# Kernel tuning notes

Measured on AMD Instinct MI355X. Metric: run time of the kernel, lower is better.

The kernel has to match this reference:

```python
import jax, jax.numpy as jnp
import numpy as np

IN_COUNT, OUT_COUNT, NUM_BASIS = 512, 512, 8
X_MIN, X_MAX, GAMMA_SCALE = 0.0, 1.0, 3.0
BATCH = 8192


def setup_inputs() -> dict:
    key = jax.random.key(0)
    k_x, k_c = jax.random.split(key)
    x = jax.random.uniform(k_x, (BATCH, IN_COUNT), dtype=jnp.float32)
    coeffs = 0.01 * jax.random.normal(k_c, (OUT_COUNT, IN_COUNT, NUM_BASIS), dtype=jnp.float32)
    centers_1d = jnp.linspace(X_MIN, X_MAX, NUM_BASIS, dtype=jnp.float32)
    centers = jnp.tile(centers_1d[None, :], (IN_COUNT, 1))  # (in, basis)
    delta = (X_MAX - X_MIN) / (NUM_BASIS - 1)
    gamma = GAMMA_SCALE / delta
    slopes = jnp.full((IN_COUNT, NUM_BASIS), gamma, dtype=jnp.float32)
    return {"x": x, "coeffs": coeffs, "centers": centers, "slopes": slopes}


def reference(x, coeffs, centers, slopes):
    # s_im(x) = 0.5 * (1 + tanh(gamma_im * (x_bi - c_im)))  -> (batch, in, basis)
    basis = 0.5 * (1.0 + jnp.tanh(slopes[None, :, :] * (x[:, :, None] - centers[None, :, :])))
    # y_bj = sum_{i,m} a_jim * s_bim : fused double reduction (GEMM-shaped)
    y = jnp.einsum('bim,jim->bj', basis, coeffs)
    return y
```

## Files before the change

### kernel.cpp

```cpp
#include <hip/hip_runtime.h>

#define BATCH 8192
#define INC   512
#define OUTC  512
#define NB    8
#define KDIM  (INC * NB)

#define BM 128
#define BN 128
#define BK 64
#define KSPLIT 2
#define THREADS 256
#define LDA 72

typedef __attribute__((ext_vector_type(8))) short bf16x8;
typedef __attribute__((ext_vector_type(4))) float f32x4;
typedef __attribute__((ext_vector_type(4))) int   i32x4;

static __device__ __forceinline__ unsigned int pk2(float lo, float hi) {
    return __builtin_amdgcn_perm(__builtin_bit_cast(unsigned int, hi),
                                 __builtin_bit_cast(unsigned int, lo),
                                 0x07060302u);
}

__global__ __launch_bounds__(256)
void w_prepass(const float* __restrict__ W, unsigned short* __restrict__ Wb,
               float* __restrict__ Y) {
    const int gid  = blockIdx.x * 256 + threadIdx.x;
    const int base = gid * 8;
    const float4 a = *(const float4*)(W + base);
    const float4 b = *(const float4*)(W + base + 4);
    const float v[8] = {a.x, a.y, a.z, a.w, b.x, b.y, b.z, b.w};
    unsigned int r[8];
#pragma unroll
    for (int i = 0; i < 8; ++i) {
        unsigned int t = __builtin_bit_cast(unsigned int, v[i]);
        t += 0x7FFFu + ((t >> 16) & 1u);
        r[i] = t >> 16;
    }
    i32x4 out = {(int)(r[0] | (r[1] << 16)), (int)(r[2] | (r[3] << 16)),
                 (int)(r[4] | (r[5] << 16)), (int)(r[6] | (r[7] << 16))};
    *(i32x4*)(Wb + base) = out;

    float4* yp = (float4*)Y + (size_t)gid * 4;
    const float4 z = {0.f, 0.f, 0.f, 0.f};
#pragma unroll
    for (int i = 0; i < 4; ++i) yp[i] = z;
}


template <bool DMA, bool SPLIT>
__global__ __launch_bounds__(THREADS, 2)
void tanh_basis_fused_gemm(const float* __restrict__ X,
                           const void*  __restrict__ Wsrc,
                           const float* __restrict__ CEN,
                           const float* __restrict__ SLP,
                           float* __restrict__ Y)
{
    __shared__ short As[2][BM][LDA];
    __shared__ short Bs[2][BN * BK];

    const int tid  = threadIdx.x;
    const int lane = tid & 63;
    const int wave = tid >> 6;
    const int wm   = wave & 1;
    const int wn   = wave >> 1;

    const int b0 = blockIdx.x * BM;
    const int j0 = blockIdx.y * BN;
    constexpr int NKTB = SPLIT ? (KDIM / BK / KSPLIT) : (KDIM / BK);
    const int kt0 = SPLIT ? blockIdx.z * NKTB : 0;

    const float L2E = 1.4426950408889634f;
    const float g2  = 2.0f * SLP[0] * L2E;
    const float pc  = -g2;
    const float q0  = g2 * CEN[0];
    const float R   = __builtin_amdgcn_exp2f(g2 * (CEN[1] - CEN[0]));

    const int arow  = tid >> 1;
    const int aquad = tid & 1;
    const float* xp = X + (size_t)(b0 + arow) * INC + aquad * 4;

    f32x4 acc[4][4];
#pragma unroll
    for (int i = 0; i < 4; ++i)
#pragma unroll
        for (int j = 0; j < 4; ++j)
            acc[i][j] = (f32x4){0.f, 0.f, 0.f, 0.f};

    const int rl = lane & 15;
    const int h  = lane >> 4;
    const int aoff = (wm * 64 + rl) * LDA + h * 8;
    const int brow = wn * 64 + rl;
    const int low3 = lane & 7;
    const int boff0 = brow * BK + ((h)     ^ low3) * 8;
    const int boff1 = brow * BK + ((4 + h) ^ low3) * 8;

    const int dma_r    = lane >> 3;
    const int dma_kblk = (lane & 7) ^ dma_r;

    auto stage_B = [&](int ktA, short* bs) {
        if constexpr (DMA) {
            const unsigned short* Wb = (const unsigned short*)Wsrc;
#pragma unroll
            for (int q = 0; q < 4; ++q) {
                const int cc = wave * 4 + q;
                const unsigned short* gp = Wb
                    + (size_t)(j0 + cc * 8 + dma_r) * KDIM
                    + ktA * BK + dma_kblk * 8;
                __builtin_amdgcn_global_load_lds(
                    (const __attribute__((address_space(1))) void*)gp,
                    (__attribute__((address_space(3))) void*)(bs + cc * 512),
                    16, 0, 0);
            }
        } else {
            const float* Wf = (const float*)Wsrc;
            const int frow = tid >> 1;
            const int fkh  = tid & 1;
            const float* wp = Wf + (size_t)(j0 + frow) * KDIM + ktA * BK + fkh * 32;
            float4 cv[8];
#pragma unroll
            for (int q = 0; q < 8; ++q) cv[q] = ((const float4*)wp)[q];
#pragma unroll
            for (int kb = 0; kb < 4; ++kb) {
                const int kblk = fkh * 4 + kb;
                i32x4* bw = (i32x4*)(bs + frow * BK + ((kblk ^ (frow & 7)) * 8));
                *bw = (i32x4){(int)pk2(cv[2*kb].x, cv[2*kb].y),
                              (int)pk2(cv[2*kb].z, cv[2*kb].w),
                              (int)pk2(cv[2*kb+1].x, cv[2*kb+1].y),
                              (int)pk2(cv[2*kb+1].z, cv[2*kb+1].w)};
            }
        }
    };

    auto octet_i = [&](float x) -> i32x4 {
        float e = __builtin_amdgcn_exp2f(fmaf(pc, x, q0));
        float s[NB];
#pragma unroll
        for (int m = 0; m < NB; ++m) {
            s[m] = __builtin_amdgcn_rcpf(1.0f + e);
            e *= R;
        }
        return (i32x4){(int)pk2(s[0], s[1]), (int)pk2(s[2], s[3]),
                       (int)pk2(s[4], s[5]), (int)pk2(s[6], s[7])};
    };

    auto stage_A = [&](float4 xq, short* as_base) {
        short* ap = as_base + arow * LDA + aquad * 32;
        *(i32x4*)(ap)      = octet_i(xq.x);
        *(i32x4*)(ap + 8)  = octet_i(xq.y);
        *(i32x4*)(ap + 16) = octet_i(xq.z);
        *(i32x4*)(ap + 24) = octet_i(xq.w);
    };

    float4 xv = *(const float4*)(xp + (size_t)kt0 * 8);
    stage_B(kt0, &Bs[0][0]);
    stage_A(xv, &As[0][0][0]);
    xv = *(const float4*)(xp + (size_t)(kt0 + 1) * 8);
    float4 xn;

#define STEP(RT, CUR, NXT)                                                   \
    {                                                                        \
        const int rn_ = ((RT) + 1 < NKTB) ? (RT) + 1 : NKTB - 1;             \
        const int rx_ = ((RT) + 2 < NKTB) ? (RT) + 2 : NKTB - 1;             \
        xn = *(const float4*)(xp + (size_t)(kt0 + rx_) * 8);                 \
        stage_B(kt0 + rn_, &Bs[NXT][0]);                                     \
        stage_A(xv, &As[NXT][0][0]);                                         \
        __builtin_amdgcn_sched_barrier(0);                                   \
        asm volatile("s_waitcnt vmcnt(5) lgkmcnt(0)" ::: "memory");          \
        __builtin_amdgcn_s_barrier();                                        \
        __builtin_amdgcn_sched_barrier(0);                                   \
        const short* abase = &As[CUR][0][0];                                 \
        const short* bbase = &Bs[CUR][0];                                    \
        bf16x8 af[2][4], bfr[2][4];                                          \
        _Pragma("unroll") for (int ks = 0; ks < 2; ++ks) {                   \
            _Pragma("unroll") for (int mf = 0; mf < 4; ++mf)                 \
                af[ks][mf] = *(const bf16x8*)(abase + aoff                   \
                                              + mf * (16 * LDA) + ks * 32);  \
            const int boffk = ks ? boff1 : boff0;                            \
            _Pragma("unroll") for (int nf = 0; nf < 4; ++nf)                 \
                bfr[ks][nf] = *(const bf16x8*)(bbase + boffk                 \
                                               + nf * (16 * BK));            \
        }                                                                    \
        __builtin_amdgcn_s_setprio(1);                                       \
        _Pragma("unroll") for (int ks = 0; ks < 2; ++ks)                     \
            _Pragma("unroll") for (int mf = 0; mf < 4; ++mf)                 \
                _Pragma("unroll") for (int nf = 0; nf < 4; ++nf)             \
                    acc[mf][nf] = __builtin_amdgcn_mfma_f32_16x16x32_bf16(   \
                        af[ks][mf], bfr[ks][nf], acc[mf][nf], 0, 0, 0);      \
        __builtin_amdgcn_s_setprio(0);                                       \
        __builtin_amdgcn_sched_barrier(0);                                   \
        __builtin_amdgcn_s_barrier();                                        \
        xv = xn;                                                             \
    }

    static_assert(NKTB % 2 == 0, "dbuf unroll");
    for (int t = 0; t < NKTB; t += 2) {
        STEP(t,     0, 1)
        STEP(t + 1, 1, 0)
    }
#undef STEP

    asm volatile("s_waitcnt vmcnt(0) lgkmcnt(0)" ::: "memory");

    const int rowb = b0 + wm * 64 + h * 4;
    const int colb = j0 + wn * 64 + rl;
#pragma unroll
    for (int mf = 0; mf < 4; ++mf)
#pragma unroll
        for (int nf = 0; nf < 4; ++nf)
#pragma unroll
            for (int rr = 0; rr < 4; ++rr) {
                const size_t idx = (size_t)(rowb + mf * 16 + rr) * OUTC
                                 + (colb + nf * 16);
                if constexpr (SPLIT)
                    unsafeAtomicAdd(&Y[idx], acc[mf][nf][rr]);
                else
                    Y[idx] = acc[mf][nf][rr];
            }
}

extern "C" void kernel_launch(void* const* d_in, const int* in_sizes, int n_in,
                              void* d_out, int out_size, void* d_ws, size_t ws_size,
                              hipStream_t stream) {
    const float* X   = (const float*)d_in[0];
    const float* W   = (const float*)d_in[1];
    const float* CEN = (const float*)d_in[2];
    const float* SLP = (const float*)d_in[3];
    float* Y = (float*)d_out;

    static_assert(BATCH % BM == 0 && OUTC % BN == 0 && KDIM % (BK * KSPLIT) == 0,
                  "tiling");

    const size_t WB_BYTES = (size_t)OUTC * KDIM * sizeof(unsigned short);
    if (ws_size >= WB_BYTES) {
        w_prepass<<<dim3((OUTC * KDIM) / (8 * 256)), dim3(256), 0, stream>>>(
            W, (unsigned short*)d_ws, Y);
        dim3 grid(BATCH / BM, OUTC / BN, KSPLIT);
        tanh_basis_fused_gemm<true, true><<<grid, dim3(THREADS), 0, stream>>>(
            X, d_ws, CEN, SLP, Y);
    } else {
        dim3 grid(BATCH / BM, OUTC / BN, 1);
        tanh_basis_fused_gemm<false, false><<<grid, dim3(THREADS), 0, stream>>>(
            X, (const void*)W, CEN, SLP, Y);
    }
}
```

Baseline: 142.4 us.

## Halve M tile, raise occupancy, interleave basis staging between MFMA halves

Shrinks the block M tile from 128 to 64 rows, so each thread computes two basis octets per step instead of four and each wave holds a 2x4 accumulator grid. Launch bounds go to three blocks per CU. The next-tile A basis computation (exp2/rcp) now sits between the two k-substeps of MFMAs instead of before the barrier, so transcendental work can overlap matrix instructions, and the setprio and sched_barrier hints are dropped. This trades lower per-block arithmetic intensity and twice as many B tile loads per output for more occupancy and overlap.

Measured after the change: 150.8 us. 5.9% more time.

```diff
diff --git a/kernel.cpp b/kernel.cpp
--- a/kernel.cpp
+++ b/kernel.cpp
@@ -6,7 +6,7 @@
 #define NB    8
 #define KDIM  (INC * NB)
 
-#define BM 128
+#define BM 64
 #define BN 128
 #define BK 64
 #define KSPLIT 2
@@ -50,7 +50,7 @@
 
 
 template <bool DMA, bool SPLIT>
-__global__ __launch_bounds__(THREADS, 2)
+__global__ __launch_bounds__(THREADS, 3)
 void tanh_basis_fused_gemm(const float* __restrict__ X,
                            const void*  __restrict__ Wsrc,
                            const float* __restrict__ CEN,
@@ -77,22 +77,22 @@
     const float q0  = g2 * CEN[0];
     const float R   = __builtin_amdgcn_exp2f(g2 * (CEN[1] - CEN[0]));
 
-    const int arow  = tid >> 1;
-    const int aquad = tid & 1;
-    const float* xp = X + (size_t)(b0 + arow) * INC + aquad * 4;
-
-    f32x4 acc[4][4];
-#pragma unroll
-    for (int i = 0; i < 4; ++i)
+    const int arow = tid >> 2;
+    const int acol = (tid & 3) * 2;
+    const float* xp = X + (size_t)(b0 + arow) * INC + acol;
+
+    f32x4 acc[2][4];
+#pragma unroll
+    for (int i = 0; i < 2; ++i)
 #pragma unroll
         for (int j = 0; j < 4; ++j)
             acc[i][j] = (f32x4){0.f, 0.f, 0.f, 0.f};
 
     const int rl = lane & 15;
     const int h  = lane >> 4;
-    const int aoff = (wm * 64 + rl) * LDA + h * 8;
-    const int brow = wn * 64 + rl;
-    const int low3 = lane & 7;
+    const int aoff  = (wm * 32 + rl) * LDA + h * 8;
+    const int brow  = wn * 64 + rl;
+    const int low3  = lane & 7;
     const int boff0 = brow * BK + ((h)     ^ low3) * 8;
     const int boff1 = brow * BK + ((4 + h) ^ low3) * 8;
 
@@ -145,36 +145,31 @@
                        (int)pk2(s[4], s[5]), (int)pk2(s[6], s[7])};
     };
 
-    auto stage_A = [&](float4 xq, short* as_base) {
-        short* ap = as_base + arow * LDA + aquad * 32;
-        *(i32x4*)(ap)      = octet_i(xq.x);
-        *(i32x4*)(ap + 8)  = octet_i(xq.y);
-        *(i32x4*)(ap + 16) = octet_i(xq.z);
-        *(i32x4*)(ap + 24) = octet_i(xq.w);
+    auto stage_A = [&](float2 xq, short* as_base) {
+        short* ap = as_base + arow * LDA + acol * 8;
+        *(i32x4*)(ap)     = octet_i(xq.x);
+        *(i32x4*)(ap + 8) = octet_i(xq.y);
     };
 
-    float4 xv = *(const float4*)(xp + (size_t)kt0 * 8);
+    float2 xv = *(const float2*)(xp + (size_t)kt0 * NB);
     stage_B(kt0, &Bs[0][0]);
     stage_A(xv, &As[0][0][0]);
-    xv = *(const float4*)(xp + (size_t)(kt0 + 1) * 8);
-    float4 xn;
+    xv = *(const float2*)(xp + (size_t)(kt0 + 1) * NB);
+    float2 xn;
 
 #define STEP(RT, CUR, NXT)                                                   \
     {                                                                        \
         const int rn_ = ((RT) + 1 < NKTB) ? (RT) + 1 : NKTB - 1;             \
         const int rx_ = ((RT) + 2 < NKTB) ? (RT) + 2 : NKTB - 1;             \
-        xn = *(const float4*)(xp + (size_t)(kt0 + rx_) * 8);                 \
+        xn = *(const float2*)(xp + (size_t)(kt0 + rx_) * NB);                \
         stage_B(kt0 + rn_, &Bs[NXT][0]);                                     \
-        stage_A(xv, &As[NXT][0][0]);                                         \
-        __builtin_amdgcn_sched_barrier(0);                                   \
         asm volatile("s_waitcnt vmcnt(5) lgkmcnt(0)" ::: "memory");          \
         __builtin_amdgcn_s_barrier();                                        \
-        __builtin_amdgcn_sched_barrier(0);                                   \
         const short* abase = &As[CUR][0][0];                                 \
         const short* bbase = &Bs[CUR][0];                                    \
-        bf16x8 af[2][4], bfr[2][4];                                          \
+        bf16x8 af[2][2], bfr[2][4];                                          \
         _Pragma("unroll") for (int ks = 0; ks < 2; ++ks) {                   \
-            _Pragma("unroll") for (int mf = 0; mf < 4; ++mf)                 \
+            _Pragma("unroll") for (int mf = 0; mf < 2; ++mf)                 \
                 af[ks][mf] = *(const bf16x8*)(abase + aoff                   \
                                               + mf * (16 * LDA) + ks * 32);  \
             const int boffk = ks ? boff1 : boff0;                            \
@@ -182,14 +177,15 @@
                 bfr[ks][nf] = *(const bf16x8*)(bbase + boffk                 \
                                                + nf * (16 * BK));            \
         }                                                                    \
-        __builtin_amdgcn_s_setprio(1);                                       \
-        _Pragma("unroll") for (int ks = 0; ks < 2; ++ks)                     \
-            _Pragma("unroll") for (int mf = 0; mf < 4; ++mf)                 \
-                _Pragma("unroll") for (int nf = 0; nf < 4; ++nf)             \
-                    acc[mf][nf] = __builtin_amdgcn_mfma_f32_16x16x32_bf16(   \
-                        af[ks][mf], bfr[ks][nf], acc[mf][nf], 0, 0, 0);      \
-        __builtin_amdgcn_s_setprio(0);                                       \
-        __builtin_amdgcn_sched_barrier(0);                                   \
+        _Pragma("unroll") for (int mf = 0; mf < 2; ++mf)                     \
+            _Pragma("unroll") for (int nf = 0; nf < 4; ++nf)                 \
+                acc[mf][nf] = __builtin_amdgcn_mfma_f32_16x16x32_bf16(       \
+                    af[0][mf], bfr[0][nf], acc[mf][nf], 0, 0, 0);            \
+        stage_A(xv, &As[NXT][0][0]);        \
+        _Pragma("unroll") for (int mf = 0; mf < 2; ++mf)                     \
+            _Pragma("unroll") for (int nf = 0; nf < 4; ++nf)                 \
+                acc[mf][nf] = __builtin_amdgcn_mfma_f32_16x16x32_bf16(       \
+                    af[1][mf], bfr[1][nf], acc[mf][nf], 0, 0, 0);            \
         __builtin_amdgcn_s_barrier();                                        \
         xv = xn;                                                             \
     }
@@ -203,10 +199,10 @@
 
     asm volatile("s_waitcnt vmcnt(0) lgkmcnt(0)" ::: "memory");
 
-    const int rowb = b0 + wm * 64 + h * 4;
+    const int rowb = b0 + wm * 32 + h * 4;
     const int colb = j0 + wn * 64 + rl;
 #pragma unroll
-    for (int mf = 0; mf < 4; ++mf)
+    for (int mf = 0; mf < 2; ++mf)
 #pragma unroll
         for (int nf = 0; nf < 4; ++nf)
 #pragma unroll
```
